# Optimization experiments

Hardware: AMD Instinct MI355X
Metric: run time of the kernel (lower is better)

Reference implementation:

```python
import jax, jax.numpy as jnp
import numpy as np
from functools import partial

VOCAB = 32000
EMBED = 512
HIDDEN = 1024
NUM_LAYERS = 2
REP_PENALTY = 1.2
BATCH, SEQ = 64, 128


def _lstm_layer(xs, w_ih, w_hh, b_ih, b_hh):
    """PyTorch-convention LSTM layer. xs: [B,T,D_in] -> hs: [B,T,H].
    Gate order i,f,g,o; weights [4H, D_in]/[4H, H]."""
    B = xs.shape[0]
    H = w_hh.shape[1]
    # precompute input projections for all timesteps: [B,T,4H]
    x_proj = jnp.einsum('btd,gd->btg', xs, w_ih) + b_ih + b_hh

    def step(carry, xp):
        h, c = carry
        gates = xp + h @ w_hh.T  # [B,4H]
        i, f, g, o = jnp.split(gates, 4, axis=-1)
        i = jax.nn.sigmoid(i)
        f = jax.nn.sigmoid(f)
        g = jnp.tanh(g)
        o = jax.nn.sigmoid(o)
        c = f * c + i * g
        h = o * jnp.tanh(c)
        return (h, c), h

    h0 = jnp.zeros((B, H), xs.dtype)
    c0 = jnp.zeros((B, H), xs.dtype)
    _, hs = jax.lax.scan(step, (h0, c0), x_proj.transpose(1, 0, 2))  # [T,B,H]
    return hs.transpose(1, 0, 2)


def setup_inputs() -> dict:
    key = jax.random.key(0)
    ks = jax.random.split(key, 16)
    s_emb = 1.0  # nn.Embedding default init ~ N(0,1)
    x = jax.random.randint(ks[0], (BATCH, SEQ), 0, VOCAB, dtype=jnp.int32)
    emb = jax.random.normal(ks[1], (VOCAB, EMBED), jnp.float32) * s_emb

    def lstm_params(k, d_in):
        k1, k2, k3, k4 = jax.random.split(k, 4)
        s = 1.0 / np.sqrt(HIDDEN)
        return (
            jax.random.uniform(k1, (4 * HIDDEN, d_in), jnp.float32, -s, s),
            jax.random.uniform(k2, (4 * HIDDEN, HIDDEN), jnp.float32, -s, s),
            jax.random.uniform(k3, (4 * HIDDEN,), jnp.float32, -s, s),
            jax.random.uniform(k4, (4 * HIDDEN,), jnp.float32, -s, s),
        )

    w_ih0, w_hh0, b_ih0, b_hh0 = lstm_params(ks[2], EMBED)
    w_ih1, w_hh1, b_ih1, b_hh1 = lstm_params(ks[3], HIDDEN)
    s_fc = 1.0 / np.sqrt(HIDDEN)
    fc_w = jax.random.uniform(ks[4], (VOCAB, HIDDEN), jnp.float32, -s_fc, s_fc)
    fc_b = jax.random.uniform(ks[5], (VOCAB,), jnp.float32, -s_fc, s_fc)
    return {
        'x': x, 'emb': emb,
        'w_ih0': w_ih0, 'w_hh0': w_hh0, 'b_ih0': b_ih0, 'b_hh0': b_hh0,
        'w_ih1': w_ih1, 'w_hh1': w_hh1, 'b_ih1': b_ih1, 'b_hh1': b_hh1,
        'fc_w': fc_w, 'fc_b': fc_b,
    }


def reference(x, emb, w_ih0, w_hh0, b_ih0, b_hh0,
              w_ih1, w_hh1, b_ih1, b_hh1, fc_w, fc_b):
    h = emb[x]                                          # [B,S,E] embedding lookup
    h = _lstm_layer(h, w_ih0, w_hh0, b_ih0, b_hh0)      # [B,S,H]
    h = _lstm_layer(h, w_ih1, w_hh1, b_ih1, b_hh1)      # [B,S,H]
    last = h[:, -1, :]                                  # [B,H]
    out = last @ fc_w.T + fc_b                          # [B,V]
    # repetition penalty: each occurrence of token t in row i divides out[i,t]
    # by the penalty once => out[i,t] /= penalty**count(t in x[i]).
    B = x.shape[0]
    rows = jnp.broadcast_to(jnp.arange(B)[:, None], x.shape)
    counts = jnp.zeros((B, VOCAB), out.dtype).at[rows, x].add(1.0)
    out = out / jnp.power(jnp.asarray(REP_PENALTY, out.dtype), counts)
    return out
```

## Files before the change

kernel.cpp:

```cpp
#include <hip/hip_runtime.h>
#include <hip/hip_bf16.h>
#include <stdint.h>

#define NB 64
#define NT 128
#define NE 512
#define NH 1024
#define NV 32000
#define NM (NB*NT)
#define NBNH (NB*NH)

#define NWG 256
#define NTH 512
#define FLAG_STRIDE 32u

#define HSLOT_B (NB*NH*2u)
#define WS_FLAGS   0u
#define WS_FLAG_B  (NWG*FLAG_STRIDE*4u)
#define WS_H0      WS_FLAG_B
#define WS_H1      (WS_H0 + 129u*HSLOT_B)
#define WS_CNT     (WS_H1 + 129u*HSLOT_B)
#define WS_XS0     (WS_CNT + 4u*NB*NV)
#define WS_NEEDED  (WS_XS0 + 2u*NM*NE)

typedef __attribute__((ext_vector_type(8))) short bf16x8;
typedef __attribute__((ext_vector_type(4))) float f32x4;

#define SCOPE_AG  __HIP_MEMORY_SCOPE_AGENT

__device__ __forceinline__ unsigned short f2bf(float f) {
  unsigned u = __float_as_uint(f);
  u += 0x7FFFu + ((u >> 16) & 1u);
  return (unsigned short)(u >> 16);
}
__device__ __forceinline__ float sigmoidf_(float x) {
  return 1.0f / (1.0f + expf(-x));
}
__device__ __forceinline__ bf16x8 pack8(float4 a, float4 b) {
  bf16x8 v;
  v[0]=(short)f2bf(a.x); v[1]=(short)f2bf(a.y); v[2]=(short)f2bf(a.z); v[3]=(short)f2bf(a.w);
  v[4]=(short)f2bf(b.x); v[5]=(short)f2bf(b.y); v[6]=(short)f2bf(b.z); v[7]=(short)f2bf(b.w);
  return v;
}

template <int SLP>
__device__ __forceinline__ void gbar_light(unsigned* flags, unsigned n) {
  __syncthreads();
  if (threadIdx.x == 0)
    __hip_atomic_store(&flags[(unsigned)blockIdx.x * FLAG_STRIDE], n,
                       __ATOMIC_RELAXED, SCOPE_AG);
  if (threadIdx.x < NWG) {
    while (__hip_atomic_load(&flags[(unsigned)threadIdx.x * FLAG_STRIDE],
                             __ATOMIC_RELAXED, SCOPE_AG) < n)
      __builtin_amdgcn_s_sleep(SLP);
  }
  __syncthreads();
}

#define MFMA(a,b,c) __builtin_amdgcn_mfma_f32_16x16x32_bf16((a),(b),(c),0,0,0)

__global__ void __launch_bounds__(NTH, 2)
lstm_all(const int* __restrict__ x, const float* __restrict__ emb,
         const float* __restrict__ w_ih0, const float* __restrict__ w_hh0,
         const float* __restrict__ b_ih0, const float* __restrict__ b_hh0,
         const float* __restrict__ w_ih1, const float* __restrict__ w_hh1,
         const float* __restrict__ b_ih1, const float* __restrict__ b_hh1,
         const float* __restrict__ fc_w, const float* __restrict__ fc_b,
         float* __restrict__ out, unsigned char* __restrict__ wsb)
{
  __shared__ unsigned short sWih1[32*64*8];
  __shared__ unsigned short sWih0[16*64*8];
  __shared__ float sG0[NB][16], sGih[NB][16], sG1a[NB][16], sG1b[NB][16];
  __shared__ float sB0[16], sB1[16];
  __shared__ alignas(8) unsigned short sH0[NB][4], sH1[NB][4];

  const int wg  = blockIdx.x;
  const int tid = threadIdx.x;
  const int wave = tid >> 6, lane = tid & 63;
  const int lr = lane & 15, lq = lane >> 4;

  unsigned* flags = (unsigned*)(wsb + WS_FLAGS);
  unsigned short* hist0 = (unsigned short*)(wsb + WS_H0);
  unsigned short* hist1 = (unsigned short*)(wsb + WS_H1);
  unsigned* counts = (unsigned*)(wsb + WS_CNT);
  unsigned short* xs0 = (unsigned short*)(wsb + WS_XS0);

  const int gr = (lr >> 2)*NH + wg*4 + (lr & 3);

  const unsigned kkw = (unsigned)wg >> 3, lqw = ((unsigned)wg >> 1) & 3, j0 = ((unsigned)wg & 1)*4;
  const size_t pubOff = ((size_t)((lane>>4)*32 + kkw)*64 + lqw*16 + (lane&15))*8 + j0;

  bf16x8 breg[32];
  {
    const float* wsrc = (wave < 4 ? w_hh0 : w_hh1) + (size_t)gr*NH + lq*8;
    #pragma unroll
    for (int kk = 0; kk < 32; ++kk)
      breg[kk] = pack8(*(const float4*)(wsrc + kk*32), *(const float4*)(wsrc + kk*32 + 4));
  }

  for (int i = wg*NTH + tid; i < NM*(NE/8); i += NWG*NTH) {
    int m = i >> 6;
    int e8 = (i & 63) << 3;
    int t = m >> 6, b = m & 63;
    int tok = x[b*NT + t];
    const float* s = emb + (size_t)tok*NE + e8;
    union { bf16x8 v8; unsigned long long u[2]; } u;
    u.v8 = pack8(*(const float4*)s, *(const float4*)(s + 4));
    int mblk = m >> 4, lrm = m & 15;
    int kk = e8 >> 5, lqm = (e8 >> 3) & 3;
    size_t elem = ((size_t)(mblk*16 + kk)*64 + lqm*16 + lrm) * 8;
    unsigned long long* dst = (unsigned long long*)(xs0 + elem);
    __hip_atomic_store(dst,   u.u[0], __ATOMIC_RELAXED, SCOPE_AG);
    __hip_atomic_store(dst+1, u.u[1], __ATOMIC_RELAXED, SCOPE_AG);
  }

  for (int i = tid; i < 32*64; i += NTH) {
    int kk = i >> 6, l = i & 63;
    int glr = l & 15, glq = l >> 4;
    int ggr = (glr >> 2)*NH + wg*4 + (glr & 3);
    const float* p = w_ih1 + (size_t)ggr*NH + kk*32 + glq*8;
    ((bf16x8*)sWih1)[i] = pack8(*(const float4*)p, *(const float4*)(p + 4));
  }
  for (int i = tid; i < 16*64; i += NTH) {
    int kk = i >> 6, l = i & 63;
    int glr = l & 15, glq = l >> 4;
    int ggr = (glr >> 2)*NH + wg*4 + (glr & 3);
    const float* p = w_ih0 + (size_t)ggr*NE + kk*32 + glq*8;
    ((bf16x8*)sWih0)[i] = pack8(*(const float4*)p, *(const float4*)(p + 4));
  }
  if (tid < 16) {
    int g2 = (tid >> 2)*NH + wg*4 + (tid & 3);
    sB0[tid] = b_ih0[g2] + b_hh0[g2];
    sB1[tid] = b_ih1[g2] + b_hh1[g2];
  }
  {
    int i = wg*NTH + tid;
    if (i < NB*NT) {
      int b = i >> 7;
      atomicAdd(&counts[(size_t)b*NV + x[i]], 1u);
    }
  }
  unsigned bar = 1;
  gbar_light<8>(flags, bar);

  if (wave >= 4) {
    const unsigned short* X = xs0 + ((size_t)(0*4 + (wave-4))*1024 + lane)*8;
    f32x4 ai = {0.f,0.f,0.f,0.f};
    #pragma unroll
    for (int kk = 0; kk < 16; ++kk)
      ai = MFMA(*(const bf16x8*)(X + kk*512), ((const bf16x8*)sWih0)[kk*64 + lane], ai);
    #pragma unroll
    for (int r = 0; r < 4; ++r) sGih[(wave-4)*16 + lq*4 + r][lr] = ai[r];
  }

  float c_reg = 0.f;
  const int cb = (tid & 255) >> 2, cu = tid & 3;
  for (int t = 0; t <= NT; ++t) {
    if (wave < 4) {
      const unsigned short* A = hist0 + (size_t)t*NBNH + (size_t)(wave*2048 + lane)*8;
      f32x4 a0 = {0.f,0.f,0.f,0.f}, a1 = {0.f,0.f,0.f,0.f};
      #pragma unroll
      for (int kk = 0; kk < 32; ++kk) {
        bf16x8 af = *(const bf16x8*)(A + kk*512);
        a0 = MFMA(af, breg[kk], a0);
        a1 = MFMA(af, ((const bf16x8*)sWih1)[kk*64 + lane], a1);
      }
      #pragma unroll
      for (int r = 0; r < 4; ++r) {
        sG0 [wave*16 + lq*4 + r][lr] = a0[r];
        sG1a[wave*16 + lq*4 + r][lr] = a1[r];
      }
    } else {
      if (t >= 1) {
        const unsigned short* A = hist1 + (size_t)(t-1)*NBNH + (size_t)((wave-4)*2048 + lane)*8;
        f32x4 a2 = {0.f,0.f,0.f,0.f};
        #pragma unroll
        for (int kk = 0; kk < 32; ++kk)
          a2 = MFMA(*(const bf16x8*)(A + kk*512), breg[kk], a2);
        #pragma unroll
        for (int r = 0; r < 4; ++r) sG1b[(wave-4)*16 + lq*4 + r][lr] = a2[r];
      }
    }
    __syncthreads();
    if (tid < 256) {
      if (t < NT) {
        float gi = sG0[cb][cu]    + sGih[cb][cu]    + sB0[cu];
        float gf = sG0[cb][4+cu]  + sGih[cb][4+cu]  + sB0[4+cu];
        float gg = sG0[cb][8+cu]  + sGih[cb][8+cu]  + sB0[8+cu];
        float go = sG0[cb][12+cu] + sGih[cb][12+cu] + sB0[12+cu];
        float ii = sigmoidf_(gi), ff = sigmoidf_(gf), g = tanhf(gg), oo = sigmoidf_(go);
        c_reg = ff*c_reg + ii*g;
        sH0[cb][cu] = f2bf(oo * tanhf(c_reg));
      }
    } else {
      if (t >= 1) {
        float gi = sG1a[cb][cu]    + sG1b[cb][cu]    + sB1[cu];
        float gf = sG1a[cb][4+cu]  + sG1b[cb][4+cu]  + sB1[4+cu];
        float gg = sG1a[cb][8+cu]  + sG1b[cb][8+cu]  + sB1[8+cu];
        float go = sG1a[cb][12+cu] + sG1b[cb][12+cu] + sB1[12+cu];
        float ii = sigmoidf_(gi), ff = sigmoidf_(gf), g = tanhf(gg), oo = sigmoidf_(go);
        c_reg = ff*c_reg + ii*g;
        sH1[cb][cu] = f2bf(oo * tanhf(c_reg));
      }
    }
    __syncthreads();
    if (wave == 0 && t < NT) {
      unsigned long long v = *(const unsigned long long*)&sH0[lane][0];
      __hip_atomic_store((unsigned long long*)(hist0 + (size_t)(t+1)*NBNH + pubOff),
                         v, __ATOMIC_RELAXED, SCOPE_AG);
    }
    if (wave == 1 && t >= 1) {
      unsigned long long v = *(const unsigned long long*)&sH1[lane][0];
      __hip_atomic_store((unsigned long long*)(hist1 + (size_t)t*NBNH + pubOff),
                         v, __ATOMIC_RELAXED, SCOPE_AG);
    }
    if (wave >= 4 && (t + 1) < NT) {
      const unsigned short* X = xs0 + ((size_t)((t+1)*4 + (wave-4))*1024 + lane)*8;
      f32x4 ai = {0.f,0.f,0.f,0.f};
      #pragma unroll
      for (int kk = 0; kk < 16; ++kk)
        ai = MFMA(*(const bf16x8*)(X + kk*512), ((const bf16x8*)sWih0)[kk*64 + lane], ai);
      #pragma unroll
      for (int r = 0; r < 4; ++r) sGih[(wave-4)*16 + lq*4 + r][lr] = ai[r];
    }
    gbar_light<4>(flags, ++bar);
  }

  {
    const unsigned short* ab = hist1 + (size_t)128*NBNH + (size_t)lane*8;
    int tile = wg*8 + wave;
    if (tile < NV/16) {
      int c0 = tile*16;
      const float* wb = fc_w + (size_t)(c0 + lr)*NH + lq*8;
      f32x4 acc[4] = {{0.f,0.f,0.f,0.f},{0.f,0.f,0.f,0.f},{0.f,0.f,0.f,0.f},{0.f,0.f,0.f,0.f}};
      #pragma unroll 4
      for (int kk = 0; kk < 32; ++kk) {
        bf16x8 bfv = pack8(*(const float4*)(wb + kk*32), *(const float4*)(wb + kk*32 + 4));
        #pragma unroll
        for (int mt = 0; mt < 4; ++mt) {
          bf16x8 af = *(const bf16x8*)(ab + (size_t)(mt*32 + kk)*512);
          acc[mt] = MFMA(af, bfv, acc[mt]);
        }
      }
      int c = c0 + lr;
      float fb = fc_b[c];
      #pragma unroll
      for (int mt = 0; mt < 4; ++mt) {
        #pragma unroll
        for (int r = 0; r < 4; ++r) {
          int b = mt*16 + lq*4 + r;
          unsigned cnt = counts[(size_t)b*NV + c];
          float v = (acc[mt][r] + fb) * exp2f(-0.26303440583379378f * (float)cnt);
          out[(size_t)b*NV + c] = v;
        }
      }
    }
  }
}

extern "C" void kernel_launch(void* const* d_in, const int* in_sizes, int n_in,
                              void* d_out, int out_size, void* d_ws, size_t ws_size,
                              hipStream_t stream) {
  const int*   x     = (const int*)  d_in[0];
  const float* emb   = (const float*)d_in[1];
  const float* w_ih0 = (const float*)d_in[2];
  const float* w_hh0 = (const float*)d_in[3];
  const float* b_ih0 = (const float*)d_in[4];
  const float* b_hh0 = (const float*)d_in[5];
  const float* w_ih1 = (const float*)d_in[6];
  const float* w_hh1 = (const float*)d_in[7];
  const float* b_ih1 = (const float*)d_in[8];
  const float* b_hh1 = (const float*)d_in[9];
  const float* fc_w  = (const float*)d_in[10];
  const float* fc_b  = (const float*)d_in[11];
  if (ws_size < WS_NEEDED) return;
  unsigned char* ws = (unsigned char*)d_ws;
  (void)hipMemsetAsync(ws + WS_FLAGS, 0, WS_FLAG_B, stream);
  (void)hipMemsetAsync(ws + WS_H0, 0, 2u*129u*HSLOT_B, stream);
  (void)hipMemsetAsync(ws + WS_CNT, 0, 4u*NB*NV, stream);
  hipLaunchKernelGGL(lstm_all, dim3(NWG), dim3(NTH), 0, stream,
                     x, emb, w_ih0, w_hh0, b_ih0, b_hh0,
                     w_ih1, w_hh1, b_ih1, b_hh1, fc_w, fc_b,
                     (float*)d_out, (unsigned char*)d_ws);
}
```

Before: 1.113 ms.

## Use sharded atomic-counter grid barrier and publish hidden state directly from cell threads

```diff
diff --git a/kernel.cpp b/kernel.cpp
--- a/kernel.cpp
+++ b/kernel.cpp
@@ -15,9 +15,9 @@
 #define FLAG_STRIDE 32u
 
 #define HSLOT_B (NB*NH*2u)
-#define WS_FLAGS   0u
-#define WS_FLAG_B  (NWG*FLAG_STRIDE*4u)
-#define WS_H0      WS_FLAG_B
+#define WS_CNTR    0u
+#define WS_CNTR_B  (NWG*FLAG_STRIDE*4u)
+#define WS_H0      WS_CNTR_B
 #define WS_H1      (WS_H0 + 129u*HSLOT_B)
 #define WS_CNT     (WS_H1 + 129u*HSLOT_B)
 #define WS_XS0     (WS_CNT + 4u*NB*NV)
@@ -44,14 +44,14 @@
 }
 
 template <int SLP>
-__device__ __forceinline__ void gbar_light(unsigned* flags, unsigned n) {
+__device__ __forceinline__ void gbar_cnt(unsigned* cnt, unsigned bar) {
   __syncthreads();
   if (threadIdx.x == 0)
-    __hip_atomic_store(&flags[(unsigned)blockIdx.x * FLAG_STRIDE], n,
-                       __ATOMIC_RELAXED, SCOPE_AG);
-  if (threadIdx.x < NWG) {
-    while (__hip_atomic_load(&flags[(unsigned)threadIdx.x * FLAG_STRIDE],
-                             __ATOMIC_RELAXED, SCOPE_AG) < n)
+    __hip_atomic_fetch_add(&cnt[((unsigned)blockIdx.x & 7u) * FLAG_STRIDE], 1u,
+                           __ATOMIC_RELAXED, SCOPE_AG);
+  if (threadIdx.x >= 64 && threadIdx.x < 72) {
+    while (__hip_atomic_load(&cnt[((unsigned)threadIdx.x - 64u) * FLAG_STRIDE],
+                             __ATOMIC_RELAXED, SCOPE_AG) < 32u * bar)
       __builtin_amdgcn_s_sleep(SLP);
   }
   __syncthreads();
@@ -72,14 +72,13 @@
   __shared__ unsigned short sWih0[16*64*8];
   __shared__ float sG0[NB][16], sGih[NB][16], sG1a[NB][16], sG1b[NB][16];
   __shared__ float sB0[16], sB1[16];
-  __shared__ alignas(8) unsigned short sH0[NB][4], sH1[NB][4];
 
   const int wg  = blockIdx.x;
   const int tid = threadIdx.x;
   const int wave = tid >> 6, lane = tid & 63;
   const int lr = lane & 15, lq = lane >> 4;
 
-  unsigned* flags = (unsigned*)(wsb + WS_FLAGS);
+  unsigned* cntr = (unsigned*)(wsb + WS_CNTR);
   unsigned short* hist0 = (unsigned short*)(wsb + WS_H0);
   unsigned short* hist1 = (unsigned short*)(wsb + WS_H1);
   unsigned* counts = (unsigned*)(wsb + WS_CNT);
@@ -88,7 +87,8 @@
   const int gr = (lr >> 2)*NH + wg*4 + (lr & 3);
 
   const unsigned kkw = (unsigned)wg >> 3, lqw = ((unsigned)wg >> 1) & 3, j0 = ((unsigned)wg & 1)*4;
-  const size_t pubOff = ((size_t)((lane>>4)*32 + kkw)*64 + lqw*16 + (lane&15))*8 + j0;
+  const int cb = (tid & 255) >> 2, cu = tid & 3;
+  const size_t elemB = ((size_t)((cb >> 4)*32 + kkw)*64 + lqw*16 + (cb & 15))*8 + j0;
 
   bf16x8 breg[32];
   {
@@ -141,34 +141,31 @@
     }
   }
   unsigned bar = 1;
-  gbar_light<8>(flags, bar);
-
-  if (wave >= 4) {
-    const unsigned short* X = xs0 + ((size_t)(0*4 + (wave-4))*1024 + lane)*8;
-    f32x4 ai = {0.f,0.f,0.f,0.f};
-    #pragma unroll
-    for (int kk = 0; kk < 16; ++kk)
-      ai = MFMA(*(const bf16x8*)(X + kk*512), ((const bf16x8*)sWih0)[kk*64 + lane], ai);
-    #pragma unroll
-    for (int r = 0; r < 4; ++r) sGih[(wave-4)*16 + lq*4 + r][lr] = ai[r];
-  }
+  gbar_cnt<8>(cntr, bar);
 
   float c_reg = 0.f;
-  const int cb = (tid & 255) >> 2, cu = tid & 3;
   for (int t = 0; t <= NT; ++t) {
     if (wave < 4) {
       const unsigned short* A = hist0 + (size_t)t*NBNH + (size_t)(wave*2048 + lane)*8;
       f32x4 a0 = {0.f,0.f,0.f,0.f}, a1 = {0.f,0.f,0.f,0.f};
-      #pragma unroll
-      for (int kk = 0; kk < 32; ++kk) {
-        bf16x8 af = *(const bf16x8*)(A + kk*512);
-        a0 = MFMA(af, breg[kk], a0);
-        a1 = MFMA(af, ((const bf16x8*)sWih1)[kk*64 + lane], a1);
-      }
-      #pragma unroll
-      for (int r = 0; r < 4; ++r) {
-        sG0 [wave*16 + lq*4 + r][lr] = a0[r];
-        sG1a[wave*16 + lq*4 + r][lr] = a1[r];
+      if (t < NT) {
+        #pragma unroll
+        for (int kk = 0; kk < 32; ++kk) {
+          bf16x8 af = *(const bf16x8*)(A + kk*512);
+          a0 = MFMA(af, breg[kk], a0);
+          a1 = MFMA(af, ((const bf16x8*)sWih1)[kk*64 + lane], a1);
+        }
+        #pragma unroll
+        for (int r = 0; r < 4; ++r) {
+          sG0 [wave*16 + lq*4 + r][lr] = a0[r];
+          sG1a[wave*16 + lq*4 + r][lr] = a1[r];
+        }
+      } else {
+        #pragma unroll
+        for (int kk = 0; kk < 32; ++kk)
+          a1 = MFMA(*(const bf16x8*)(A + kk*512), ((const bf16x8*)sWih1)[kk*64 + lane], a1);
+        #pragma unroll
+        for (int r = 0; r < 4; ++r) sG1a[wave*16 + lq*4 + r][lr] = a1[r];
       }
     } else {
       if (t >= 1) {
@@ -179,6 +176,15 @@
           a2 = MFMA(*(const bf16x8*)(A + kk*512), breg[kk], a2);
         #pragma unroll
         for (int r = 0; r < 4; ++r) sG1b[(wave-4)*16 + lq*4 + r][lr] = a2[r];
+      }
+      if (t < NT) {
+        const unsigned short* X = xs0 + ((size_t)(t*4 + (wave-4))*1024 + lane)*8;
+        f32x4 ai = {0.f,0.f,0.f,0.f};
+        #pragma unroll
+        for (int kk = 0; kk < 16; ++kk)
+          ai = MFMA(*(const bf16x8*)(X + kk*512), ((const bf16x8*)sWih0)[kk*64 + lane], ai);
+        #pragma unroll
+        for (int r = 0; r < 4; ++r) sGih[(wave-4)*16 + lq*4 + r][lr] = ai[r];
       }
     }
     __syncthreads();
@@ -190,7 +196,16 @@
         float go = sG0[cb][12+cu] + sGih[cb][12+cu] + sB0[12+cu];
         float ii = sigmoidf_(gi), ff = sigmoidf_(gf), g = tanhf(gg), oo = sigmoidf_(go);
         c_reg = ff*c_reg + ii*g;
-        sH0[cb][cu] = f2bf(oo * tanhf(c_reg));
+        unsigned hb = f2bf(oo * tanhf(c_reg));
+        unsigned o1 = (unsigned)__shfl_down((int)hb, 1);
+        unsigned o2 = (unsigned)__shfl_down((int)hb, 2);
+        unsigned o3 = (unsigned)__shfl_down((int)hb, 3);
+        if (cu == 0) {
+          unsigned long long v = (unsigned long long)(hb | (o1 << 16))
+                               | ((unsigned long long)(o2 | (o3 << 16)) << 32);
+          __hip_atomic_store((unsigned long long*)(hist0 + (size_t)(t+1)*NBNH + elemB),
+                             v, __ATOMIC_RELAXED, SCOPE_AG);
+        }
       }
     } else {
       if (t >= 1) {
@@ -200,30 +215,19 @@
         float go = sG1a[cb][12+cu] + sG1b[cb][12+cu] + sB1[12+cu];
         float ii = sigmoidf_(gi), ff = sigmoidf_(gf), g = tanhf(gg), oo = sigmoidf_(go);
         c_reg = ff*c_reg + ii*g;
-        sH1[cb][cu] = f2bf(oo * tanhf(c_reg));
-      }
-    }
-    __syncthreads();
-    if (wave == 0 && t < NT) {
-      unsigned long long v = *(const unsigned long long*)&sH0[lane][0];
-      __hip_atomic_store((unsigned long long*)(hist0 + (size_t)(t+1)*NBNH + pubOff),
-                         v, __ATOMIC_RELAXED, SCOPE_AG);
-    }
-    if (wave == 1 && t >= 1) {
-      unsigned long long v = *(const unsigned long long*)&sH1[lane][0];
-      __hip_atomic_store((unsigned long long*)(hist1 + (size_t)t*NBNH + pubOff),
-                         v, __ATOMIC_RELAXED, SCOPE_AG);
-    }
-    if (wave >= 4 && (t + 1) < NT) {
-      const unsigned short* X = xs0 + ((size_t)((t+1)*4 + (wave-4))*1024 + lane)*8;
-      f32x4 ai = {0.f,0.f,0.f,0.f};
-      #pragma unroll
-      for (int kk = 0; kk < 16; ++kk)
-        ai = MFMA(*(const bf16x8*)(X + kk*512), ((const bf16x8*)sWih0)[kk*64 + lane], ai);
-      #pragma unroll
-      for (int r = 0; r < 4; ++r) sGih[(wave-4)*16 + lq*4 + r][lr] = ai[r];
-    }
-    gbar_light<4>(flags, ++bar);
+        unsigned hb = f2bf(oo * tanhf(c_reg));
+        unsigned o1 = (unsigned)__shfl_down((int)hb, 1);
+        unsigned o2 = (unsigned)__shfl_down((int)hb, 2);
+        unsigned o3 = (unsigned)__shfl_down((int)hb, 3);
+        if (cu == 0) {
+          unsigned long long v = (unsigned long long)(hb | (o1 << 16))
+                               | ((unsigned long long)(o2 | (o3 << 16)) << 32);
+          __hip_atomic_store((unsigned long long*)(hist1 + (size_t)t*NBNH + elemB),
+                             v, __ATOMIC_RELAXED, SCOPE_AG);
+        }
+      }
+    }
+    gbar_cnt<4>(cntr, ++bar);
   }
 
   {
@@ -275,8 +279,9 @@
   const float* fc_b  = (const float*)d_in[11];
   if (ws_size < WS_NEEDED) return;
   unsigned char* ws = (unsigned char*)d_ws;
-  (void)hipMemsetAsync(ws + WS_FLAGS, 0, WS_FLAG_B, stream);
-  (void)hipMemsetAsync(ws + WS_H0, 0, 2u*129u*HSLOT_B, stream);
+  (void)hipMemsetAsync(ws + WS_CNTR, 0, WS_CNTR_B, stream);
+  (void)hipMemsetAsync(ws + WS_H0, 0, HSLOT_B, stream);
+  (void)hipMemsetAsync(ws + WS_H1, 0, HSLOT_B, stream);
   (void)hipMemsetAsync(ws + WS_CNT, 0, 4u*NB*NV, stream);
   hipLaunchKernelGGL(lstm_all, dim3(NWG), dim3(NTH), 0, stream,
                      x, emb, w_ih0, w_hh0, b_ih0, b_hh0,
```

New measurement: 1.078 ms. 3.1% less time.

## Split batch into two independent workgroup groups with per-group barriers

Applied to the files above, without the earlier changes.

```diff
diff --git a/kernel.cpp b/kernel.cpp
--- a/kernel.cpp
+++ b/kernel.cpp
@@ -8,18 +8,19 @@
 #define NH 1024
 #define NV 32000
 #define NM (NB*NT)
-#define NBNH (NB*NH)
 
 #define NWG 256
 #define NTH 512
+#define WPG 128
 #define FLAG_STRIDE 32u
 
-#define HSLOT_B (NB*NH*2u)
-#define WS_FLAGS   0u
-#define WS_FLAG_B  (NWG*FLAG_STRIDE*4u)
-#define WS_H0      WS_FLAG_B
-#define WS_H1      (WS_H0 + 129u*HSLOT_B)
-#define WS_CNT     (WS_H1 + 129u*HSLOT_B)
+#define HS_SHORTS 32768u
+#define GSTRIDE_SH (129u*HS_SHORTS)
+#define WS_FLAGS_S 0u
+#define WS_FLAGS_G 32768u
+#define WS_H0      65536u
+#define WS_H1      (WS_H0 + 2u*129u*65536u)
+#define WS_CNT     (WS_H1 + 2u*129u*65536u)
 #define WS_XS0     (WS_CNT + 4u*NB*NV)
 #define WS_NEEDED  (WS_XS0 + 2u*NM*NE)
 
@@ -41,20 +42,6 @@
   v[0]=(short)f2bf(a.x); v[1]=(short)f2bf(a.y); v[2]=(short)f2bf(a.z); v[3]=(short)f2bf(a.w);
   v[4]=(short)f2bf(b.x); v[5]=(short)f2bf(b.y); v[6]=(short)f2bf(b.z); v[7]=(short)f2bf(b.w);
   return v;
-}
-
-template <int SLP>
-__device__ __forceinline__ void gbar_light(unsigned* flags, unsigned n) {
-  __syncthreads();
-  if (threadIdx.x == 0)
-    __hip_atomic_store(&flags[(unsigned)blockIdx.x * FLAG_STRIDE], n,
-                       __ATOMIC_RELAXED, SCOPE_AG);
-  if (threadIdx.x < NWG) {
-    while (__hip_atomic_load(&flags[(unsigned)threadIdx.x * FLAG_STRIDE],
-                             __ATOMIC_RELAXED, SCOPE_AG) < n)
-      __builtin_amdgcn_s_sleep(SLP);
-  }
-  __syncthreads();
 }
 
 #define MFMA(a,b,c) __builtin_amdgcn_mfma_f32_16x16x32_bf16((a),(b),(c),0,0,0)
@@ -68,34 +55,50 @@
          const float* __restrict__ fc_w, const float* __restrict__ fc_b,
          float* __restrict__ out, unsigned char* __restrict__ wsb)
 {
-  __shared__ unsigned short sWih1[32*64*8];
-  __shared__ unsigned short sWih0[16*64*8];
-  __shared__ float sG0[NB][16], sGih[NB][16], sG1a[NB][16], sG1b[NB][16];
-  __shared__ float sB0[16], sB1[16];
-  __shared__ alignas(8) unsigned short sH0[NB][4], sH1[NB][4];
+  __shared__ unsigned short sWih1[2*32*64*8];
+  __shared__ unsigned short sWhh0c1[32*64*8];
+  __shared__ unsigned short sWhh1c1[32*64*8];
+  __shared__ float sG0[32][32], sG1a[32][32], sG1b[32][32], sGih[32][32];
+  __shared__ float sB0[32], sB1[32];
+  __shared__ alignas(16) unsigned short sH0[32][8], sH1[32][8];
 
   const int wg  = blockIdx.x;
   const int tid = threadIdx.x;
   const int wave = tid >> 6, lane = tid & 63;
   const int lr = lane & 15, lq = lane >> 4;
-
-  unsigned* flags = (unsigned*)(wsb + WS_FLAGS);
-  unsigned short* hist0 = (unsigned short*)(wsb + WS_H0);
-  unsigned short* hist1 = (unsigned short*)(wsb + WS_H1);
+  const int g  = wg >> 7;
+  const int wgl = wg & 127;
+
+  unsigned* flagsS = (unsigned*)(wsb + WS_FLAGS_S);
+  unsigned* gf     = (unsigned*)(wsb + WS_FLAGS_G) + (unsigned)g*WPG*FLAG_STRIDE;
+  unsigned short* h0g = (unsigned short*)(wsb + WS_H0) + (size_t)g*GSTRIDE_SH;
+  unsigned short* h1g = (unsigned short*)(wsb + WS_H1) + (size_t)g*GSTRIDE_SH;
   unsigned* counts = (unsigned*)(wsb + WS_CNT);
   unsigned short* xs0 = (unsigned short*)(wsb + WS_XS0);
 
-  const int gr = (lr >> 2)*NH + wg*4 + (lr & 3);
-
-  const unsigned kkw = (unsigned)wg >> 3, lqw = ((unsigned)wg >> 1) & 3, j0 = ((unsigned)wg & 1)*4;
-  const size_t pubOff = ((size_t)((lane>>4)*32 + kkw)*64 + lqw*16 + (lane&15))*8 + j0;
-
   bf16x8 breg[32];
   {
-    const float* wsrc = (wave < 4 ? w_hh0 : w_hh1) + (size_t)gr*NH + lq*8;
-    #pragma unroll
-    for (int kk = 0; kk < 32; ++kk)
-      breg[kk] = pack8(*(const float4*)(wsrc + kk*32), *(const float4*)(wsrc + kk*32 + 4));
+    const int ggr0 = (lr >> 3)*NH + wgl*8 + (lr & 7);
+    const int ggr1 = (2 + (lr >> 3))*NH + wgl*8 + (lr & 7);
+    if (wave == 2 || wave == 3) {
+      const float* src = w_hh0 + (size_t)ggr0*NH + lq*8;
+      #pragma unroll
+      for (int kk = 0; kk < 32; ++kk)
+        breg[kk] = pack8(*(const float4*)(src + kk*32), *(const float4*)(src + kk*32 + 4));
+    } else if (wave == 0 || wave == 1) {
+      const float* src = w_hh1 + (size_t)ggr0*NH + lq*8;
+      #pragma unroll
+      for (int kk = 0; kk < 32; ++kk)
+        breg[kk] = pack8(*(const float4*)(src + kk*32), *(const float4*)(src + kk*32 + 4));
+    } else if (wave == 4 || wave == 5) {
+      const float* s0 = w_ih0 + (size_t)ggr0*NE + lq*8;
+      const float* s1 = w_ih0 + (size_t)ggr1*NE + lq*8;
+      #pragma unroll
+      for (int kk = 0; kk < 16; ++kk) {
+        breg[kk]    = pack8(*(const float4*)(s0 + kk*32), *(const float4*)(s0 + kk*32 + 4));
+        breg[16+kk] = pack8(*(const float4*)(s1 + kk*32), *(const float4*)(s1 + kk*32 + 4));
+      }
+    }
   }
 
   for (int i = wg*NTH + tid; i < NM*(NE/8); i += NWG*NTH) {
@@ -106,30 +109,33 @@
     const float* s = emb + (size_t)tok*NE + e8;
     union { bf16x8 v8; unsigned long long u[2]; } u;
     u.v8 = pack8(*(const float4*)s, *(const float4*)(s + 4));
-    int mblk = m >> 4, lrm = m & 15;
-    int kk = e8 >> 5, lqm = (e8 >> 3) & 3;
-    size_t elem = ((size_t)(mblk*16 + kk)*64 + lqm*16 + lrm) * 8;
-    unsigned long long* dst = (unsigned long long*)(xs0 + elem);
+    int gg = b >> 5, bb = b & 31;
+    size_t off = ((size_t)((gg*NT + t)*2 + (bb >> 4)))*8192
+               + ((size_t)((e8 >> 5)*64 + ((e8 >> 3) & 3)*16 + (bb & 15)))*8;
+    unsigned long long* dst = (unsigned long long*)(xs0 + off);
     __hip_atomic_store(dst,   u.u[0], __ATOMIC_RELAXED, SCOPE_AG);
     __hip_atomic_store(dst+1, u.u[1], __ATOMIC_RELAXED, SCOPE_AG);
   }
 
+  for (int i = tid; i < 2*32*64; i += NTH) {
+    int ct = i >> 11, kk = (i >> 6) & 31, l = i & 63;
+    int glr = l & 15, glq = l >> 4;
+    int c = ct*16 + glr;
+    int ggr = (c >> 3)*NH + wgl*8 + (c & 7);
+    const float* p = w_ih1 + (size_t)ggr*NH + kk*32 + glq*8;
+    ((bf16x8*)sWih1)[i] = pack8(*(const float4*)p, *(const float4*)(p + 4));
+  }
   for (int i = tid; i < 32*64; i += NTH) {
     int kk = i >> 6, l = i & 63;
     int glr = l & 15, glq = l >> 4;
-    int ggr = (glr >> 2)*NH + wg*4 + (glr & 3);
-    const float* p = w_ih1 + (size_t)ggr*NH + kk*32 + glq*8;
-    ((bf16x8*)sWih1)[i] = pack8(*(const float4*)p, *(const float4*)(p + 4));
-  }
-  for (int i = tid; i < 16*64; i += NTH) {
-    int kk = i >> 6, l = i & 63;
-    int glr = l & 15, glq = l >> 4;
-    int ggr = (glr >> 2)*NH + wg*4 + (glr & 3);
-    const float* p = w_ih0 + (size_t)ggr*NE + kk*32 + glq*8;
-    ((bf16x8*)sWih0)[i] = pack8(*(const float4*)p, *(const float4*)(p + 4));
-  }
-  if (tid < 16) {
-    int g2 = (tid >> 2)*NH + wg*4 + (tid & 3);
+    int ggr = (2 + (glr >> 3))*NH + wgl*8 + (glr & 7);
+    const float* p0 = w_hh0 + (size_t)ggr*NH + kk*32 + glq*8;
+    const float* p1 = w_hh1 + (size_t)ggr*NH + kk*32 + glq*8;
+    ((bf16x8*)sWhh0c1)[i] = pack8(*(const float4*)p0, *(const float4*)(p0 + 4));
+    ((bf16x8*)sWhh1c1)[i] = pack8(*(const float4*)p1, *(const float4*)(p1 + 4));
+  }
+  if (tid < 32) {
+    int g2 = (tid >> 3)*NH + wgl*8 + (tid & 7);
     sB0[tid] = b_ih0[g2] + b_hh0[g2];
     sB1[tid] = b_ih1[g2] + b_hh1[g2];
   }
@@ -140,119 +146,147 @@
       atomicAdd(&counts[(size_t)b*NV + x[i]], 1u);
     }
   }
-  unsigned bar = 1;
-  gbar_light<8>(flags, bar);
-
-  if (wave >= 4) {
-    const unsigned short* X = xs0 + ((size_t)(0*4 + (wave-4))*1024 + lane)*8;
-    f32x4 ai = {0.f,0.f,0.f,0.f};
-    #pragma unroll
-    for (int kk = 0; kk < 16; ++kk)
-      ai = MFMA(*(const bf16x8*)(X + kk*512), ((const bf16x8*)sWih0)[kk*64 + lane], ai);
-    #pragma unroll
-    for (int r = 0; r < 4; ++r) sGih[(wave-4)*16 + lq*4 + r][lr] = ai[r];
-  }
+  __syncthreads();
+  if (tid == 0)
+    __hip_atomic_store(&flagsS[(unsigned)wg * FLAG_STRIDE], 1u, __ATOMIC_RELAXED, SCOPE_AG);
+  if (tid < NWG) {
+    while (__hip_atomic_load(&flagsS[(unsigned)tid * FLAG_STRIDE], __ATOMIC_RELAXED, SCOPE_AG) < 1u)
+      __builtin_amdgcn_s_sleep(8);
+  }
+  __syncthreads();
 
   float c_reg = 0.f;
-  const int cb = (tid & 255) >> 2, cu = tid & 3;
+  const int cbb = (tid & 255) >> 3, cu8 = tid & 7;
   for (int t = 0; t <= NT; ++t) {
-    if (wave < 4) {
-      const unsigned short* A = hist0 + (size_t)t*NBNH + (size_t)(wave*2048 + lane)*8;
-      f32x4 a0 = {0.f,0.f,0.f,0.f}, a1 = {0.f,0.f,0.f,0.f};
+    if (wave == 2 || wave == 3) {
+      const int rb = wave - 2;
+      const unsigned short* A = h0g + (size_t)t*HS_SHORTS + rb*16384 + lane*8;
+      f32x4 a00 = {0.f,0.f,0.f,0.f}, a01 = {0.f,0.f,0.f,0.f};
+      f32x4 a10 = {0.f,0.f,0.f,0.f}, a11 = {0.f,0.f,0.f,0.f};
       #pragma unroll
       for (int kk = 0; kk < 32; ++kk) {
         bf16x8 af = *(const bf16x8*)(A + kk*512);
-        a0 = MFMA(af, breg[kk], a0);
-        a1 = MFMA(af, ((const bf16x8*)sWih1)[kk*64 + lane], a1);
+        a00 = MFMA(af, breg[kk], a00);
+        a01 = MFMA(af, ((const bf16x8*)sWhh0c1)[kk*64 + lane], a01);
+        a10 = MFMA(af, ((const bf16x8*)sWih1)[kk*64 + lane], a10);
+        a11 = MFMA(af, ((const bf16x8*)sWih1)[(32+kk)*64 + lane], a11);
       }
       #pragma unroll
       for (int r = 0; r < 4; ++r) {
-        sG0 [wave*16 + lq*4 + r][lr] = a0[r];
-        sG1a[wave*16 + lq*4 + r][lr] = a1[r];
-      }
-    } else {
+        int row = rb*16 + lq*4 + r;
+        sG0 [row][lr]    = a00[r];
+        sG0 [row][16+lr] = a01[r];
+        sG1a[row][lr]    = a10[r];
+        sG1a[row][16+lr] = a11[r];
+      }
+    } else if (wave == 0 || wave == 1) {
       if (t >= 1) {
-        const unsigned short* A = hist1 + (size_t)(t-1)*NBNH + (size_t)((wave-4)*2048 + lane)*8;
-        f32x4 a2 = {0.f,0.f,0.f,0.f};
+        const int rb = wave;
+        const unsigned short* A = h1g + (size_t)(t-1)*HS_SHORTS + rb*16384 + lane*8;
+        f32x4 a20 = {0.f,0.f,0.f,0.f}, a21 = {0.f,0.f,0.f,0.f};
         #pragma unroll
-        for (int kk = 0; kk < 32; ++kk)
-          a2 = MFMA(*(const bf16x8*)(A + kk*512), breg[kk], a2);
+        for (int kk = 0; kk < 32; ++kk) {
+          bf16x8 af = *(const bf16x8*)(A + kk*512);
+          a20 = MFMA(af, breg[kk], a20);
+          a21 = MFMA(af, ((const bf16x8*)sWhh1c1)[kk*64 + lane], a21);
+        }
         #pragma unroll
-        for (int r = 0; r < 4; ++r) sG1b[(wave-4)*16 + lq*4 + r][lr] = a2[r];
+        for (int r = 0; r < 4; ++r) {
+          int row = rb*16 + lq*4 + r;
+          sG1b[row][lr]    = a20[r];
+          sG1b[row][16+lr] = a21[r];
+        }
+      }
+    } else if (wave == 4 || wave == 5) {
+      if (t < NT) {
+        const int rb = wave - 4;
+        const unsigned short* A = xs0 + ((size_t)((g*NT + t)*2 + rb))*8192 + lane*8;
+        f32x4 ai0 = {0.f,0.f,0.f,0.f}, ai1 = {0.f,0.f,0.f,0.f};
+        #pragma unroll
+        for (int kk = 0; kk < 16; ++kk) {
+          bf16x8 af = *(const bf16x8*)(A + kk*512);
+          ai0 = MFMA(af, breg[kk], ai0);
+          ai1 = MFMA(af, breg[16+kk], ai1);
+        }
+        #pragma unroll
+        for (int r = 0; r < 4; ++r) {
+          int row = rb*16 + lq*4 + r;
+          sGih[row][lr]    = ai0[r];
+          sGih[row][16+lr] = ai1[r];
+        }
       }
     }
     __syncthreads();
     if (tid < 256) {
       if (t < NT) {
-        float gi = sG0[cb][cu]    + sGih[cb][cu]    + sB0[cu];
-        float gf = sG0[cb][4+cu]  + sGih[cb][4+cu]  + sB0[4+cu];
-        float gg = sG0[cb][8+cu]  + sGih[cb][8+cu]  + sB0[8+cu];
-        float go = sG0[cb][12+cu] + sGih[cb][12+cu] + sB0[12+cu];
-        float ii = sigmoidf_(gi), ff = sigmoidf_(gf), g = tanhf(gg), oo = sigmoidf_(go);
-        c_reg = ff*c_reg + ii*g;
-        sH0[cb][cu] = f2bf(oo * tanhf(c_reg));
+        float gi = sG0[cbb][cu8]    + sGih[cbb][cu8]    + sB0[cu8];
+        float gf = sG0[cbb][8+cu8]  + sGih[cbb][8+cu8]  + sB0[8+cu8];
+        float gg = sG0[cbb][16+cu8] + sGih[cbb][16+cu8] + sB0[16+cu8];
+        float go = sG0[cbb][24+cu8] + sGih[cbb][24+cu8] + sB0[24+cu8];
+        float ii = sigmoidf_(gi), ff = sigmoidf_(gf), gv = tanhf(gg), oo = sigmoidf_(go);
+        c_reg = ff*c_reg + ii*gv;
+        sH0[cbb][cu8] = f2bf(oo * tanhf(c_reg));
       }
     } else {
       if (t >= 1) {
-        float gi = sG1a[cb][cu]    + sG1b[cb][cu]    + sB1[cu];
-        float gf = sG1a[cb][4+cu]  + sG1b[cb][4+cu]  + sB1[4+cu];
-        float gg = sG1a[cb][8+cu]  + sG1b[cb][8+cu]  + sB1[8+cu];
-        float go = sG1a[cb][12+cu] + sG1b[cb][12+cu] + sB1[12+cu];
-        float ii = sigmoidf_(gi), ff = sigmoidf_(gf), g = tanhf(gg), oo = sigmoidf_(go);
-        c_reg = ff*c_reg + ii*g;
-        sH1[cb][cu] = f2bf(oo * tanhf(c_reg));
+        float gi = sG1a[cbb][cu8]    + sG1b[cbb][cu8]    + sB1[cu8];
+        float gf = sG1a[cbb][8+cu8]  + sG1b[cbb][8+cu8]  + sB1[8+cu8];
+        float gg = sG1a[cbb][16+cu8] + sG1b[cbb][16+cu8] + sB1[16+cu8];
+        float go = sG1a[cbb][24+cu8] + sG1b[cbb][24+cu8] + sB1[24+cu8];
+        float ii = sigmoidf_(gi), ff = sigmoidf_(gf), gv = tanhf(gg), oo = sigmoidf_(go);
+        c_reg = ff*c_reg + ii*gv;
+        sH1[cbb][cu8] = f2bf(oo * tanhf(c_reg));
       }
     }
     __syncthreads();
-    if (wave == 0 && t < NT) {
-      unsigned long long v = *(const unsigned long long*)&sH0[lane][0];
-      __hip_atomic_store((unsigned long long*)(hist0 + (size_t)(t+1)*NBNH + pubOff),
+    if (wave == 6 && t < NT) {
+      int bb = lane >> 1, j0 = (lane & 1)*4;
+      unsigned long long v = *(const unsigned long long*)&sH0[bb][j0];
+      size_t off = ((size_t)(((bb >> 4)*32 + (wgl >> 2))*64 + (wgl & 3)*16 + (bb & 15)))*8 + j0;
+      __hip_atomic_store((unsigned long long*)(h0g + (size_t)(t+1)*HS_SHORTS + off),
                          v, __ATOMIC_RELAXED, SCOPE_AG);
     }
-    if (wave == 1 && t >= 1) {
-      unsigned long long v = *(const unsigned long long*)&sH1[lane][0];
-      __hip_atomic_store((unsigned long long*)(hist1 + (size_t)t*NBNH + pubOff),
+    if (wave == 7 && t >= 1) {
+      int bb = lane >> 1, j0 = (lane & 1)*4;
+      unsigned long long v = *(const unsigned long long*)&sH1[bb][j0];
+      size_t off = ((size_t)(((bb >> 4)*32 + (wgl >> 2))*64 + (wgl & 3)*16 + (bb & 15)))*8 + j0;
+      __hip_atomic_store((unsigned long long*)(h1g + (size_t)t*HS_SHORTS + off),
                          v, __ATOMIC_RELAXED, SCOPE_AG);
     }
-    if (wave >= 4 && (t + 1) < NT) {
-      const unsigned short* X = xs0 + ((size_t)((t+1)*4 + (wave-4))*1024 + lane)*8;
-      f32x4 ai = {0.f,0.f,0.f,0.f};
-      #pragma unroll
-      for (int kk = 0; kk < 16; ++kk)
-        ai = MFMA(*(const bf16x8*)(X + kk*512), ((const bf16x8*)sWih0)[kk*64 + lane], ai);
-      #pragma unroll
-      for (int r = 0; r < 4; ++r) sGih[(wave-4)*16 + lq*4 + r][lr] = ai[r];
-    }
-    gbar_light<4>(flags, ++bar);
+    __syncthreads();
+    if (tid == 0)
+      __hip_atomic_store(&gf[(unsigned)wgl * FLAG_STRIDE], (unsigned)(t+1),
+                         __ATOMIC_RELAXED, SCOPE_AG);
+    if (tid < WPG) {
+      while (__hip_atomic_load(&gf[(unsigned)tid * FLAG_STRIDE],
+                               __ATOMIC_RELAXED, SCOPE_AG) < (unsigned)(t+1))
+        __builtin_amdgcn_s_sleep(4);
+    }
+    __syncthreads();
   }
 
   {
-    const unsigned short* ab = hist1 + (size_t)128*NBNH + (size_t)lane*8;
-    int tile = wg*8 + wave;
-    if (tile < NV/16) {
+    const unsigned short* ab = h1g + (size_t)128*HS_SHORTS + lane*8;
+    for (int tile = wgl*8 + wave; tile < NV/16; tile += WPG*8) {
       int c0 = tile*16;
       const float* wb = fc_w + (size_t)(c0 + lr)*NH + lq*8;
-      f32x4 acc[4] = {{0.f,0.f,0.f,0.f},{0.f,0.f,0.f,0.f},{0.f,0.f,0.f,0.f},{0.f,0.f,0.f,0.f}};
+      f32x4 acc0 = {0.f,0.f,0.f,0.f}, acc1 = {0.f,0.f,0.f,0.f};
       #pragma unroll 4
       for (int kk = 0; kk < 32; ++kk) {
         bf16x8 bfv = pack8(*(const float4*)(wb + kk*32), *(const float4*)(wb + kk*32 + 4));
-        #pragma unroll
-        for (int mt = 0; mt < 4; ++mt) {
-          bf16x8 af = *(const bf16x8*)(ab + (size_t)(mt*32 + kk)*512);
-          acc[mt] = MFMA(af, bfv, acc[mt]);
-        }
+        acc0 = MFMA(*(const bf16x8*)(ab + kk*512),         bfv, acc0);
+        acc1 = MFMA(*(const bf16x8*)(ab + 16384 + kk*512), bfv, acc1);
       }
       int c = c0 + lr;
       float fb = fc_b[c];
       #pragma unroll
-      for (int mt = 0; mt < 4; ++mt) {
-        #pragma unroll
-        for (int r = 0; r < 4; ++r) {
-          int b = mt*16 + lq*4 + r;
-          unsigned cnt = counts[(size_t)b*NV + c];
-          float v = (acc[mt][r] + fb) * exp2f(-0.26303440583379378f * (float)cnt);
-          out[(size_t)b*NV + c] = v;
-        }
+      for (int r = 0; r < 4; ++r) {
+        int b0 = g*32 + lq*4 + r;
+        int b1 = b0 + 16;
+        unsigned cnt0 = counts[(size_t)b0*NV + c];
+        unsigned cnt1 = counts[(size_t)b1*NV + c];
+        out[(size_t)b0*NV + c] = (acc0[r] + fb) * exp2f(-0.26303440583379378f * (float)cnt0);
+        out[(size_t)b1*NV + c] = (acc1[r] + fb) * exp2f(-0.26303440583379378f * (float)cnt1);
       }
     }
   }
@@ -275,8 +309,11 @@
   const float* fc_b  = (const float*)d_in[11];
   if (ws_size < WS_NEEDED) return;
   unsigned char* ws = (unsigned char*)d_ws;
-  (void)hipMemsetAsync(ws + WS_FLAGS, 0, WS_FLAG_B, stream);
-  (void)hipMemsetAsync(ws + WS_H0, 0, 2u*129u*HSLOT_B, stream);
+  (void)hipMemsetAsync(ws, 0, WS_H0, stream);
+  (void)hipMemsetAsync(ws + WS_H0, 0, 65536, stream);
+  (void)hipMemsetAsync(ws + WS_H0 + 129u*65536u, 0, 65536, stream);
+  (void)hipMemsetAsync(ws + WS_H1, 0, 65536, stream);
+  (void)hipMemsetAsync(ws + WS_H1 + 129u*65536u, 0, 65536, stream);
   (void)hipMemsetAsync(ws + WS_CNT, 0, 4u*NB*NV, stream);
   hipLaunchKernelGGL(lstm_all, dim3(NWG), dim3(NTH), 0, stream,
                      x, emb, w_ih0, w_hh0, b_ih0, b_hh0,
```

Measured after the change: 991.3 us (median of 2 runs). 1.12x faster.
